# Performance work log

Measured on AMD Instinct MI355X. Metric: run time of the kernel, lower is better.

## Reference

```python
import jax, jax.numpy as jnp
import numpy as np

N_EMBD = 1024
N_HEAD = 16
B, T = 1, 4096
EPS = 1e-5


def layer_norm(x, w):
    mu = jnp.mean(x, axis=-1, keepdims=True)
    var = jnp.var(x, axis=-1, keepdims=True)
    return (x - mu) / jnp.sqrt(var + EPS) * w


def setup_inputs() -> dict:
    key = jax.random.key(0)
    ks = jax.random.split(key, 6)
    s = 0.02
    return {
        "x": jax.random.normal(ks[0], (B, T, N_EMBD), dtype=jnp.float32),
        "w_qkv": jax.random.normal(ks[1], (N_EMBD, 3 * N_EMBD), dtype=jnp.float32) * s,
        "w_attn_proj": jax.random.normal(ks[2], (N_EMBD, N_EMBD), dtype=jnp.float32) * s,
        "w_fc": jax.random.normal(ks[3], (N_EMBD, 4 * N_EMBD), dtype=jnp.float32) * s,
        "w_mlp_proj": jax.random.normal(ks[4], (4 * N_EMBD, N_EMBD), dtype=jnp.float32) * s,
        "ln1_w": jnp.ones((N_EMBD,), dtype=jnp.float32),
        "ln2_w": jnp.ones((N_EMBD,), dtype=jnp.float32),
    }


def reference(x, w_qkv, w_attn_proj, w_fc, w_mlp_proj, ln1_w, ln2_w):
    Bq, Tq, C = x.shape
    hs = C // N_HEAD

    # --- attention branch (pre-norm) ---
    h = layer_norm(x, ln1_w)
    qkv = h @ w_qkv  # [B,T,3C]
    q, k, v = jnp.split(qkv, 3, axis=-1)
    q = q.reshape(Bq, Tq, N_HEAD, hs).transpose(0, 2, 1, 3)  # [B,H,T,hs]
    k = k.reshape(Bq, Tq, N_HEAD, hs).transpose(0, 2, 1, 3)
    v = v.reshape(Bq, Tq, N_HEAD, hs).transpose(0, 2, 1, 3)

    scores = jnp.einsum("bhqd,bhkd->bhqk", q, k) * (1.0 / jnp.sqrt(jnp.float32(hs)))
    causal = jnp.tril(jnp.ones((Tq, Tq), dtype=bool))
    scores = jnp.where(causal, scores, -jnp.inf)
    weights = jax.nn.softmax(scores, axis=-1)  # dropout=0 -> identity
    out = jnp.einsum("bhqk,bhkd->bhqd", weights, v)
    out = out.transpose(0, 2, 1, 3).reshape(Bq, Tq, C)
    x = x + out @ w_attn_proj

    # --- MLP branch (pre-norm) ---
    h = layer_norm(x, ln2_w)
    h = jax.nn.gelu(h @ w_fc, approximate=False)  # nn.GELU default is exact
    x = x + h @ w_mlp_proj
    return x
```

## Files before the change

### kernel.cpp

```cpp
#include <hip/hip_runtime.h>
#include <cstdint>

typedef __attribute__((ext_vector_type(8))) short short8;
typedef __attribute__((ext_vector_type(4))) float f32x4;

__device__ __forceinline__ float b2f(unsigned short u) {
    return __uint_as_float(((unsigned int)u) << 16);
}
__device__ __forceinline__ unsigned short f2b(float f) {
    unsigned int u = __float_as_uint(f);
    u += 0x7FFFu + ((u >> 16) & 1u);
    return (unsigned short)(u >> 16);
}

__global__ __launch_bounds__(256) void k_transpose_all(
        const float* __restrict__ w0, const float* __restrict__ w1,
        const float* __restrict__ w2, const float* __restrict__ w3,
        unsigned short* __restrict__ o0, unsigned short* __restrict__ o1,
        unsigned short* __restrict__ o2, unsigned short* __restrict__ o3) {
    __shared__ float tile[32][33];
    int b = blockIdx.x;
    const float* w; unsigned short* o; int K, N, nx, tb;
    if (b < 3072)      { w = w0; o = o0; K = 1024; N = 3072; nx = 96;  tb = b; }
    else if (b < 4096) { w = w1; o = o1; K = 1024; N = 1024; nx = 32;  tb = b - 3072; }
    else if (b < 8192) { w = w2; o = o2; K = 1024; N = 4096; nx = 128; tb = b - 4096; }
    else               { w = w3; o = o3; K = 4096; N = 1024; nx = 32;  tb = b - 8192; }
    int n0 = (tb % nx) * 32, k0 = (tb / nx) * 32;
    int tx = threadIdx.x, ty = threadIdx.y;
#pragma unroll
    for (int i = 0; i < 4; i++)
        tile[ty + 8 * i][tx] = w[(size_t)(k0 + ty + 8 * i) * N + n0 + tx];
    __syncthreads();
#pragma unroll
    for (int i = 0; i < 4; i++)
        o[(size_t)(n0 + ty + 8 * i) * K + k0 + tx] = f2b(tile[tx][ty + 8 * i]);
}

__global__ __launch_bounds__(256) void k_layernorm(
        const float* __restrict__ x, const float* __restrict__ w,
        unsigned short* __restrict__ out) {
    int row = blockIdx.x, tid = threadIdx.x;
    const float4* xr = (const float4*)(x + (size_t)row * 1024);
    float4 v = xr[tid];
    float s  = v.x + v.y + v.z + v.w;
    float ss = v.x * v.x + v.y * v.y + v.z * v.z + v.w * v.w;
#pragma unroll
    for (int off = 32; off >= 1; off >>= 1) {
        s  += __shfl_down(s, off);
        ss += __shfl_down(ss, off);
    }
    __shared__ float red[10];
    if ((tid & 63) == 0) { red[tid >> 6] = s; red[4 + (tid >> 6)] = ss; }
    __syncthreads();
    if (tid == 0) {
        float S  = red[0] + red[1] + red[2] + red[3];
        float SS = red[4] + red[5] + red[6] + red[7];
        float mu  = S * (1.0f / 1024.0f);
        float var = SS * (1.0f / 1024.0f) - mu * mu;
        red[8] = mu; red[9] = rsqrtf(var + 1e-5f);
    }
    __syncthreads();
    float mu = red[8], rs = red[9];
    float4 wv = ((const float4*)w)[tid];
    ushort4 pk;
    pk.x = f2b((v.x - mu) * rs * wv.x);
    pk.y = f2b((v.y - mu) * rs * wv.y);
    pk.z = f2b((v.z - mu) * rs * wv.z);
    pk.w = f2b((v.w - mu) * rs * wv.w);
    *(ushort4*)(out + (size_t)row * 1024 + tid * 4) = pk;
}

__global__ __launch_bounds__(256) void k_reduce(
        const float* __restrict__ res, const float* __restrict__ p0,
        const float* __restrict__ p1, float* __restrict__ out, int n4) {
    int i = blockIdx.x * 256 + threadIdx.x;
    if (i < n4) {
        float4 a = ((const float4*)res)[i];
        float4 b = ((const float4*)p0)[i];
        float4 c = ((const float4*)p1)[i];
        a.x += b.x + c.x; a.y += b.y + c.y; a.z += b.z + c.z; a.w += b.w + c.w;
        ((float4*)out)[i] = a;
    }
}

template <int EPI, int TM, int TN, int MINW>
__global__ __launch_bounds__(256, MINW) void k_gemm_bt(
        const unsigned short* __restrict__ A, const unsigned short* __restrict__ BT,
        const float* __restrict__ RES, void* __restrict__ OUT,
        int M, int N, int K) {
    constexpr int WT = (TM == 128) ? 64 : 32;
    constexpr int MI = WT / 16;
    constexpr int NA = TM / 32, NB = TN / 32;
    __shared__ __align__(16) unsigned short As[TM * 64];
    __shared__ __align__(16) unsigned short Bs[TN * 64];
    int tid  = threadIdx.x;
    int lane = tid & 63, wave = tid >> 6;
    int quad = lane >> 4, qr = lane & 15;
    int wm_off = (wave >> 1) * WT;
    int wn_off = (wave & 1) * WT;
    int m0 = blockIdx.y * TM, n0 = blockIdx.x * TN;
    int ks = K / gridDim.z;
    int kbeg = blockIdx.z * ks;
    int r0 = tid >> 3;
    int c0 = (tid & 7) * 8;
    int cs = 8 * (((tid & 7) + (r0 & 7)) & 7);
    int cswz[2];
#pragma unroll
    for (int kk = 0; kk < 2; kk++) cswz[kk] = 8 * (((kk * 4) + quad + (qr & 7)) & 7);

    const unsigned short* Ap = A  + (size_t)(m0 + r0) * K + kbeg + c0;
    const unsigned short* Bp = BT + (size_t)(n0 + r0) * K + kbeg + c0;
    const size_t sA = (size_t)32 * K;

    uint4 pa0, pa1, pa2, pa3, pb0, pb1, pb2, pb3;
    pa0 = *(const uint4*)(Ap);
    pa1 = *(const uint4*)(Ap + sA);
    if constexpr (NA == 4) {
        pa2 = *(const uint4*)(Ap + 2 * sA);
        pa3 = *(const uint4*)(Ap + 3 * sA);
    }
    pb0 = *(const uint4*)(Bp);
    pb1 = *(const uint4*)(Bp + sA);
    if constexpr (NB == 4) {
        pb2 = *(const uint4*)(Bp + 2 * sA);
        pb3 = *(const uint4*)(Bp + 3 * sA);
    }

    f32x4 acc[MI][MI] = {};
    for (int k0 = 0; k0 < ks; k0 += 64) {
        __syncthreads();
        *(uint4*)&As[(r0)      * 64 + cs] = pa0;
        *(uint4*)&As[(32 + r0) * 64 + cs] = pa1;
        if constexpr (NA == 4) {
            *(uint4*)&As[(64 + r0) * 64 + cs] = pa2;
            *(uint4*)&As[(96 + r0) * 64 + cs] = pa3;
        }
        *(uint4*)&Bs[(r0)      * 64 + cs] = pb0;
        *(uint4*)&Bs[(32 + r0) * 64 + cs] = pb1;
        if constexpr (NB == 4) {
            *(uint4*)&Bs[(64 + r0) * 64 + cs] = pb2;
            *(uint4*)&Bs[(96 + r0) * 64 + cs] = pb3;
        }
        __syncthreads();
        if (k0 + 64 < ks) {
            int k = k0 + 64;
            pa0 = *(const uint4*)(Ap + k);
            pa1 = *(const uint4*)(Ap + sA + k);
            if constexpr (NA == 4) {
                pa2 = *(const uint4*)(Ap + 2 * sA + k);
                pa3 = *(const uint4*)(Ap + 3 * sA + k);
            }
            pb0 = *(const uint4*)(Bp + k);
            pb1 = *(const uint4*)(Bp + sA + k);
            if constexpr (NB == 4) {
                pb2 = *(const uint4*)(Bp + 2 * sA + k);
                pb3 = *(const uint4*)(Bp + 3 * sA + k);
            }
        }
#pragma unroll
        for (int kk = 0; kk < 2; kk++) {
            short8 af[MI], bfr[MI];
#pragma unroll
            for (int i = 0; i < MI; i++) af[i]  = *(const short8*)&As[(wm_off + i * 16 + qr) * 64 + cswz[kk]];
#pragma unroll
            for (int j = 0; j < MI; j++) bfr[j] = *(const short8*)&Bs[(wn_off + j * 16 + qr) * 64 + cswz[kk]];
#pragma unroll
            for (int i = 0; i < MI; i++)
#pragma unroll
                for (int j = 0; j < MI; j++)
                    acc[i][j] = __builtin_amdgcn_mfma_f32_16x16x32_bf16(af[i], bfr[j], acc[i][j], 0, 0, 0);
        }
    }
    float* outz = (EPI == 0) ? ((float*)OUT + (size_t)blockIdx.z * M * N) : (float*)OUT;
#pragma unroll
    for (int i = 0; i < MI; i++) {
#pragma unroll
        for (int j = 0; j < MI; j++) {
#pragma unroll
            for (int r = 0; r < 4; r++) {
                int row = m0 + wm_off + i * 16 + quad * 4 + r;
                int col = n0 + wn_off + j * 16 + qr;
                size_t idx = (size_t)row * N + col;
                float v = acc[i][j][r];
                if (EPI == 0)      outz[idx] = v;
                else if (EPI == 1) ((unsigned short*)OUT)[idx] = f2b(v);
                else if (EPI == 2) ((float*)OUT)[idx] = RES[idx] + v;
                else {
                    float u = v * fmaf(v * v, 0.035677408f, 0.79788456f);
                    float e = fminf(u * 2.885390082f, 80.0f);
                    float t = exp2f(e);
                    float g = v * t / (t + 1.0f);
                    ((unsigned short*)OUT)[idx] = f2b(g);
                }
            }
        }
    }
}

__global__ __launch_bounds__(256) void k_attn(
        const unsigned short* __restrict__ qkv, unsigned short* __restrict__ out) {
    __shared__ unsigned short Ks[128][72];
    __shared__ unsigned short Vt[64][136];
    __shared__ unsigned short Ps[4][16][136];

    const float C1 = 0.18033688f;
    const float C2 = 5.77078016f;

    int l = blockIdx.x;
    int h = l & 15;
    int qb = 63 - (l >> 4);
    int q0 = qb * 64;

    int tid = threadIdx.x;
    int wave = tid >> 6, lane = tid & 63;
    int lane16 = lane & 15, quad = lane >> 4;

    {
        int srow = tid >> 2, sc0 = (tid & 3) * 16;
        size_t base = (size_t)(q0 + srow) * 3072 + h * 64 + sc0;
        *(uint4*)&Ks[srow][sc0]     = *(const uint4*)&qkv[base];
        *(uint4*)&Ks[srow][sc0 + 8] = *(const uint4*)&qkv[base + 8];
    }
    __syncthreads();
    short8 aq0 = *(const short8*)&Ks[wave * 16 + lane16][quad * 8];
    short8 aq1 = *(const short8*)&Ks[wave * 16 + lane16][32 + quad * 8];

    f32x4 Oacc[4] = {};
    float l_part[4] = {0.f, 0.f, 0.f, 0.f};

    int srow = tid >> 1, sc0 = (tid & 1) * 32;
    int vk = (lane & 31) * 2;
    int d0 = wave * 16 + (lane >> 5) * 8;

    uint4 pk0, pk1, pk2, pk3, pv0, pv1, pv2, pv3;
    {
        size_t base = (size_t)srow * 3072 + 1024 + h * 64 + sc0;
        pk0 = *(const uint4*)&qkv[base];
        pk1 = *(const uint4*)&qkv[base + 8];
        pk2 = *(const uint4*)&qkv[base + 16];
        pk3 = *(const uint4*)&qkv[base + 24];
        size_t vb0 = (size_t)vk * 3072 + 2048 + h * 64 + d0;
        pv0 = *(const uint4*)&qkv[vb0];
        pv1 = *(const uint4*)&qkv[vb0 + 3072];
        size_t vb1 = (size_t)(64 + vk) * 3072 + 2048 + h * 64 + d0;
        pv2 = *(const uint4*)&qkv[vb1];
        pv3 = *(const uint4*)&qkv[vb1 + 3072];
    }

    for (int kc = 0; kc <= qb; kc += 2) {
        __syncthreads();
        {
            *(uint4*)&Ks[srow][sc0]      = pk0;
            *(uint4*)&Ks[srow][sc0 + 8]  = pk1;
            *(uint4*)&Ks[srow][sc0 + 16] = pk2;
            *(uint4*)&Ks[srow][sc0 + 24] = pk3;
        }
        {
            const unsigned short* pe0 = (const unsigned short*)&pv0;
            const unsigned short* po0 = (const unsigned short*)&pv1;
            const unsigned short* pe1 = (const unsigned short*)&pv2;
            const unsigned short* po1 = (const unsigned short*)&pv3;
#pragma unroll
            for (int j = 0; j < 8; j++) {
                *(uint32_t*)&Vt[d0 + j][vk]      = (uint32_t)pe0[j] | ((uint32_t)po0[j] << 16);
                *(uint32_t*)&Vt[d0 + j][64 + vk] = (uint32_t)pe1[j] | ((uint32_t)po1[j] << 16);
            }
        }
        __syncthreads();

        if (kc + 2 <= qb) {
            size_t base = (size_t)((kc + 2) * 64 + srow) * 3072 + 1024 + h * 64 + sc0;
            pk0 = *(const uint4*)&qkv[base];
            pk1 = *(const uint4*)&qkv[base + 8];
            pk2 = *(const uint4*)&qkv[base + 16];
            pk3 = *(const uint4*)&qkv[base + 24];
            size_t vb0 = (size_t)((kc + 2) * 64 + vk) * 3072 + 2048 + h * 64 + d0;
            pv0 = *(const uint4*)&qkv[vb0];
            pv1 = *(const uint4*)&qkv[vb0 + 3072];
            size_t vb1 = (size_t)((kc + 3) * 64 + vk) * 3072 + 2048 + h * 64 + d0;
            pv2 = *(const uint4*)&qkv[vb1];
            pv3 = *(const uint4*)&qkv[vb1 + 3072];
        }

        f32x4 sacc[8] = {};
#pragma unroll
        for (int kt = 0; kt < 8; kt++) {
            short8 bk0 = *(const short8*)&Ks[kt * 16 + lane16][quad * 8];
            short8 bk1 = *(const short8*)&Ks[kt * 16 + lane16][32 + quad * 8];
            sacc[kt] = __builtin_amdgcn_mfma_f32_16x16x32_bf16(aq0, bk0, sacc[kt], 0, 0, 0);
            sacc[kt] = __builtin_amdgcn_mfma_f32_16x16x32_bf16(aq1, bk1, sacc[kt], 0, 0, 0);
        }

        bool domask = (kc + 2 > qb);
#pragma unroll
        for (int r = 0; r < 4; r++) {
            int qrow = q0 + wave * 16 + quad * 4 + r;
#pragma unroll
            for (int kt = 0; kt < 8; kt++) {
                float s = sacc[kt][r];
                if (domask) {
                    int key = kc * 64 + kt * 16 + lane16;
                    s = (key <= qrow) ? s : -__builtin_inff();
                }
                float p = exp2f(fmaf(s, C1, -C2));
                l_part[r] += p;
                Ps[wave][quad * 4 + r][kt * 16 + lane16] =
                    (unsigned short)(__float_as_uint(p) >> 16);
            }
        }

#pragma unroll
        for (int s = 0; s < 4; s++) {
            short8 ap = *(const short8*)&Ps[wave][lane16][s * 32 + quad * 8];
#pragma unroll
            for (int dt = 0; dt < 4; dt++) {
                short8 bv = *(const short8*)&Vt[dt * 16 + lane16][s * 32 + quad * 8];
                Oacc[dt] = __builtin_amdgcn_mfma_f32_16x16x32_bf16(ap, bv, Oacc[dt], 0, 0, 0);
            }
        }
    }

    float invl[4];
#pragma unroll
    for (int r = 0; r < 4; r++) {
        float lf = l_part[r];
        lf += __shfl_xor(lf, 1);
        lf += __shfl_xor(lf, 2);
        lf += __shfl_xor(lf, 4);
        lf += __shfl_xor(lf, 8);
        invl[r] = 1.0f / lf;
    }
#pragma unroll
    for (int dt = 0; dt < 4; dt++) {
#pragma unroll
        for (int r = 0; r < 4; r++) {
            int qrow = q0 + wave * 16 + quad * 4 + r;
            out[(size_t)qrow * 1024 + h * 64 + dt * 16 + lane16] = f2b(Oacc[dt][r] * invl[r]);
        }
    }
}

extern "C" void kernel_launch(void* const* d_in, const int* in_sizes, int n_in,
                              void* d_out, int out_size, void* d_ws, size_t ws_size,
                              hipStream_t stream) {
    const float* x      = (const float*)d_in[0];
    const float* w_qkv  = (const float*)d_in[1];
    const float* w_attn = (const float*)d_in[2];
    const float* w_fc   = (const float*)d_in[3];
    const float* w_mlp  = (const float*)d_in[4];
    const float* ln1w   = (const float*)d_in[5];
    const float* ln2w   = (const float*)d_in[6];

    char* ws = (char*)d_ws;
    unsigned short* h      = (unsigned short*)(ws + 0);
    unsigned short* wqkvT  = (unsigned short*)(ws + 8388608);
    unsigned short* wattnT = (unsigned short*)(ws + 14680064);
    unsigned short* wfcT   = (unsigned short*)(ws + 16777216);
    unsigned short* wmlpT  = (unsigned short*)(ws + 25165824);
    unsigned short* qkv    = (unsigned short*)(ws + 33554432);
    unsigned short* attno  = (unsigned short*)(ws + 58720256);
    float*          x2     = (float*)(ws + 67108864);
    unsigned short* fcact  = (unsigned short*)(ws + 83886080);
    float* pA = (float*)(ws + 83886080);
    float* pM = (float*)(ws + 33554432);
    float* outF = (float*)d_out;

    k_transpose_all<<<12288, dim3(32, 8), 0, stream>>>(
        w_qkv, w_attn, w_fc, w_mlp, wqkvT, wattnT, wfcT, wmlpT);

    k_layernorm<<<4096, 256, 0, stream>>>(x, ln1w, h);
    k_gemm_bt<1, 128, 128, 3><<<dim3(24, 32), 256, 0, stream>>>(h, wqkvT, nullptr, qkv, 4096, 3072, 1024);
    k_attn<<<1024, 256, 0, stream>>>(qkv, attno);
    k_gemm_bt<0, 128, 128, 3><<<dim3(8, 32, 2), 256, 0, stream>>>(attno, wattnT, nullptr, pA, 4096, 1024, 1024);
    k_reduce<<<4096, 256, 0, stream>>>(x, pA, pA + 4194304, x2, 1048576);
    k_layernorm<<<4096, 256, 0, stream>>>(x2, ln2w, h);
    k_gemm_bt<3, 128, 128, 3><<<dim3(32, 32), 256, 0, stream>>>(h, wfcT, nullptr, fcact, 4096, 4096, 1024);
    k_gemm_bt<0, 128, 128, 3><<<dim3(8, 32, 2), 256, 0, stream>>>(fcact, wmlpT, nullptr, pM, 4096, 1024, 4096);
    k_reduce<<<4096, 256, 0, stream>>>(x2, pM, pM + 4194304, outF, 1048576);
}
```

Measured before the change: 356.9 us.

## Keep attention probabilities in registers by transposing QK MFMA and permuting V layout

Swaps the MFMA operands in the QK^T product so each lane holds scores for one query row across consecutive keys. The probabilities can then be packed straight into the A operand of the PV MFMA, with no round-trip through LDS. The V transpose store is permuted so its key order matches this register layout. The Ps shared buffer and its stores and reloads are removed, the row-sum reduction is simplified, and launch bounds request 4 blocks per CU. The cost is more intricate index mapping and possible register-pressure limits from the occupancy hint.

```diff
diff --git a/kernel.cpp b/kernel.cpp
--- a/kernel.cpp
+++ b/kernel.cpp
@@ -3,6 +3,7 @@
 
 typedef __attribute__((ext_vector_type(8))) short short8;
 typedef __attribute__((ext_vector_type(4))) float f32x4;
+typedef __attribute__((ext_vector_type(4))) unsigned int u32x4;
 
 __device__ __forceinline__ float b2f(unsigned short u) {
     return __uint_as_float(((unsigned int)u) << 16);
@@ -197,11 +198,10 @@
     }
 }
 
-__global__ __launch_bounds__(256) void k_attn(
+__global__ __launch_bounds__(256, 4) void k_attn(
         const unsigned short* __restrict__ qkv, unsigned short* __restrict__ out) {
     __shared__ unsigned short Ks[128][72];
     __shared__ unsigned short Vt[64][136];
-    __shared__ unsigned short Ps[4][16][136];
 
     const float C1 = 0.18033688f;
     const float C2 = 5.77078016f;
@@ -214,6 +214,7 @@
     int tid = threadIdx.x;
     int wave = tid >> 6, lane = tid & 63;
     int lane16 = lane & 15, quad = lane >> 4;
+    int qrow = q0 + wave * 16 + lane16;
 
     {
         int srow = tid >> 2, sc0 = (tid & 3) * 16;
@@ -226,11 +227,14 @@
     short8 aq1 = *(const short8*)&Ks[wave * 16 + lane16][32 + quad * 8];
 
     f32x4 Oacc[4] = {};
-    float l_part[4] = {0.f, 0.f, 0.f, 0.f};
+    float lsum = 0.f;
 
     int srow = tid >> 1, sc0 = (tid & 1) * 32;
     int vk = (lane & 31) * 2;
     int d0 = wave * 16 + (lane >> 5) * 8;
+    int u  = lane & 15;
+    int tt = ((u & 6) << 1) | ((u & 8) >> 2) | (u & 1);
+    int dstc = (lane & 16) * 2 + 2 * tt;
 
     uint4 pk0, pk1, pk2, pk3, pv0, pv1, pv2, pv3;
     {
@@ -262,8 +266,8 @@
             const unsigned short* po1 = (const unsigned short*)&pv3;
 #pragma unroll
             for (int j = 0; j < 8; j++) {
-                *(uint32_t*)&Vt[d0 + j][vk]      = (uint32_t)pe0[j] | ((uint32_t)po0[j] << 16);
-                *(uint32_t*)&Vt[d0 + j][64 + vk] = (uint32_t)pe1[j] | ((uint32_t)po1[j] << 16);
+                *(uint32_t*)&Vt[d0 + j][dstc]      = (uint32_t)pe0[j] | ((uint32_t)po0[j] << 16);
+                *(uint32_t*)&Vt[d0 + j][64 + dstc] = (uint32_t)pe1[j] | ((uint32_t)po1[j] << 16);
             }
         }
         __syncthreads();
@@ -287,55 +291,59 @@
         for (int kt = 0; kt < 8; kt++) {
             short8 bk0 = *(const short8*)&Ks[kt * 16 + lane16][quad * 8];
             short8 bk1 = *(const short8*)&Ks[kt * 16 + lane16][32 + quad * 8];
-            sacc[kt] = __builtin_amdgcn_mfma_f32_16x16x32_bf16(aq0, bk0, sacc[kt], 0, 0, 0);
-            sacc[kt] = __builtin_amdgcn_mfma_f32_16x16x32_bf16(aq1, bk1, sacc[kt], 0, 0, 0);
+            sacc[kt] = __builtin_amdgcn_mfma_f32_16x16x32_bf16(bk0, aq0, sacc[kt], 0, 0, 0);
+            sacc[kt] = __builtin_amdgcn_mfma_f32_16x16x32_bf16(bk1, aq1, sacc[kt], 0, 0, 0);
         }
 
         bool domask = (kc + 2 > qb);
-#pragma unroll
-        for (int r = 0; r < 4; r++) {
-            int qrow = q0 + wave * 16 + quad * 4 + r;
-#pragma unroll
-            for (int kt = 0; kt < 8; kt++) {
-                float s = sacc[kt][r];
-                if (domask) {
-                    int key = kc * 64 + kt * 16 + lane16;
-                    s = (key <= qrow) ? s : -__builtin_inff();
+        short8 ap[4];
+#pragma unroll
+        for (int s = 0; s < 4; s++) {
+            u32x4 w;
+#pragma unroll
+            for (int hh = 0; hh < 2; hh++) {
+                int kt = 2 * s + hh;
+                float pr[4];
+#pragma unroll
+                for (int r = 0; r < 4; r++) {
+                    float sc = sacc[kt][r];
+                    if (domask) {
+                        int key = kc * 64 + kt * 16 + quad * 4 + r;
+                        sc = (key <= qrow) ? sc : -__builtin_inff();
+                    }
+                    float p = exp2f(fmaf(sc, C1, -C2));
+                    lsum += p;
+                    pr[r] = p;
                 }
-                float p = exp2f(fmaf(s, C1, -C2));
-                l_part[r] += p;
-                Ps[wave][quad * 4 + r][kt * 16 + lane16] =
-                    (unsigned short)(__float_as_uint(p) >> 16);
-            }
+                uint32_t w0 = (__float_as_uint(pr[0]) >> 16) | (__float_as_uint(pr[1]) & 0xFFFF0000u);
+                uint32_t w1 = (__float_as_uint(pr[2]) >> 16) | (__float_as_uint(pr[3]) & 0xFFFF0000u);
+                if (hh == 0) { w.x = w0; w.y = w1; } else { w.z = w0; w.w = w1; }
+            }
+            ap[s] = __builtin_bit_cast(short8, w);
         }
 
 #pragma unroll
         for (int s = 0; s < 4; s++) {
-            short8 ap = *(const short8*)&Ps[wave][lane16][s * 32 + quad * 8];
 #pragma unroll
             for (int dt = 0; dt < 4; dt++) {
                 short8 bv = *(const short8*)&Vt[dt * 16 + lane16][s * 32 + quad * 8];
-                Oacc[dt] = __builtin_amdgcn_mfma_f32_16x16x32_bf16(ap, bv, Oacc[dt], 0, 0, 0);
-            }
-        }
-    }
-
+                Oacc[dt] = __builtin_amdgcn_mfma_f32_16x16x32_bf16(ap[s], bv, Oacc[dt], 0, 0, 0);
+            }
+        }
+    }
+
+    float lf = lsum;
+    lf += __shfl_xor(lf, 16);
+    lf += __shfl_xor(lf, 32);
     float invl[4];
 #pragma unroll
-    for (int r = 0; r < 4; r++) {
-        float lf = l_part[r];
-        lf += __shfl_xor(lf, 1);
-        lf += __shfl_xor(lf, 2);
-        lf += __shfl_xor(lf, 4);
-        lf += __shfl_xor(lf, 8);
-        invl[r] = 1.0f / lf;
-    }
+    for (int r = 0; r < 4; r++) invl[r] = 1.0f / __shfl(lf, quad * 4 + r);
 #pragma unroll
     for (int dt = 0; dt < 4; dt++) {
 #pragma unroll
         for (int r = 0; r < 4; r++) {
-            int qrow = q0 + wave * 16 + quad * 4 + r;
-            out[(size_t)qrow * 1024 + h * 64 + dt * 16 + lane16] = f2b(Oacc[dt][r] * invl[r]);
+            int qr_out = q0 + wave * 16 + quad * 4 + r;
+            out[(size_t)qr_out * 1024 + h * 64 + dt * 16 + lane16] = f2b(Oacc[dt][r] * invl[r]);
         }
     }
 }
```

After: 373.6 us. 4.7% more time.

## Split long causal attention rows across two blocks and fuse residual-reduce with layernorm

Applied to the files above, without the earlier changes.

Query blocks in the upper half of the sequence now have their key range split into two segments, each handled by its own workgroup. Each segment writes unnormalized fp32 partial outputs and row sums, and a new combine kernel merges them into bf16. This balances work across the 1536 blocks for causal attention, at the cost of extra fp32 traffic and one more launch. The residual-add reduce and the second layernorm are also fused into one kernel, which saves a launch and a re-read of x2.

```diff
diff --git a/kernel.cpp b/kernel.cpp
--- a/kernel.cpp
+++ b/kernel.cpp
@@ -68,6 +68,47 @@
     pk.z = f2b((v.z - mu) * rs * wv.z);
     pk.w = f2b((v.w - mu) * rs * wv.w);
     *(ushort4*)(out + (size_t)row * 1024 + tid * 4) = pk;
+}
+
+__global__ __launch_bounds__(256) void k_reduce_ln(
+        const float* __restrict__ res, const float* __restrict__ p0,
+        const float* __restrict__ p1, const float* __restrict__ w,
+        float* __restrict__ xout, unsigned short* __restrict__ hout) {
+    int row = blockIdx.x, tid = threadIdx.x;
+    size_t i = (size_t)row * 256 + tid;
+    float4 a = ((const float4*)res)[i];
+    float4 b = ((const float4*)p0)[i];
+    float4 c = ((const float4*)p1)[i];
+    float4 v;
+    v.x = a.x + b.x + c.x; v.y = a.y + b.y + c.y;
+    v.z = a.z + b.z + c.z; v.w = a.w + b.w + c.w;
+    ((float4*)xout)[i] = v;
+    float s  = v.x + v.y + v.z + v.w;
+    float ss = v.x * v.x + v.y * v.y + v.z * v.z + v.w * v.w;
+#pragma unroll
+    for (int off = 32; off >= 1; off >>= 1) {
+        s  += __shfl_down(s, off);
+        ss += __shfl_down(ss, off);
+    }
+    __shared__ float red[10];
+    if ((tid & 63) == 0) { red[tid >> 6] = s; red[4 + (tid >> 6)] = ss; }
+    __syncthreads();
+    if (tid == 0) {
+        float S  = red[0] + red[1] + red[2] + red[3];
+        float SS = red[4] + red[5] + red[6] + red[7];
+        float mu  = S * (1.0f / 1024.0f);
+        float var = SS * (1.0f / 1024.0f) - mu * mu;
+        red[8] = mu; red[9] = rsqrtf(var + 1e-5f);
+    }
+    __syncthreads();
+    float mu = red[8], rs = red[9];
+    float4 wv = ((const float4*)w)[tid];
+    ushort4 pk;
+    pk.x = f2b((v.x - mu) * rs * wv.x);
+    pk.y = f2b((v.y - mu) * rs * wv.y);
+    pk.z = f2b((v.z - mu) * rs * wv.z);
+    pk.w = f2b((v.w - mu) * rs * wv.w);
+    *(ushort4*)(hout + (size_t)row * 1024 + tid * 4) = pk;
 }
 
 __global__ __launch_bounds__(256) void k_reduce(
@@ -198,7 +239,8 @@
 }
 
 __global__ __launch_bounds__(256) void k_attn(
-        const unsigned short* __restrict__ qkv, unsigned short* __restrict__ out) {
+        const unsigned short* __restrict__ qkv, unsigned short* __restrict__ out,
+        float* __restrict__ pO, float* __restrict__ pL) {
     __shared__ unsigned short Ks[128][72];
     __shared__ unsigned short Vt[64][136];
     __shared__ unsigned short Ps[4][16][136];
@@ -208,8 +250,15 @@
 
     int l = blockIdx.x;
     int h = l & 15;
-    int qb = 63 - (l >> 4);
+    int u = l >> 4;
+    int k_ = u / 6, r_ = u - 6 * k_;
+    int qb, seg, split;
+    if (r_ < 4)      { qb = (r_ < 2 ? 63 : 62) - 2 * k_; seg = 1 - (r_ & 1); split = 1; }
+    else             { qb = (r_ == 4 ? 31 : 30) - 2 * k_; seg = 0; split = 0; }
     int q0 = qb * 64;
+    int nc = (qb >> 1) + 1;
+    int kcbeg = (split && seg == 1) ? 2 * (nc >> 1) : 0;
+    int kcend = (split && seg == 0) ? 2 * (nc >> 1) : 2 * nc;
 
     int tid = threadIdx.x;
     int wave = tid >> 6, lane = tid & 63;
@@ -234,20 +283,20 @@
 
     uint4 pk0, pk1, pk2, pk3, pv0, pv1, pv2, pv3;
     {
-        size_t base = (size_t)srow * 3072 + 1024 + h * 64 + sc0;
+        size_t base = (size_t)(kcbeg * 64 + srow) * 3072 + 1024 + h * 64 + sc0;
         pk0 = *(const uint4*)&qkv[base];
         pk1 = *(const uint4*)&qkv[base + 8];
         pk2 = *(const uint4*)&qkv[base + 16];
         pk3 = *(const uint4*)&qkv[base + 24];
-        size_t vb0 = (size_t)vk * 3072 + 2048 + h * 64 + d0;
+        size_t vb0 = (size_t)(kcbeg * 64 + vk) * 3072 + 2048 + h * 64 + d0;
         pv0 = *(const uint4*)&qkv[vb0];
         pv1 = *(const uint4*)&qkv[vb0 + 3072];
-        size_t vb1 = (size_t)(64 + vk) * 3072 + 2048 + h * 64 + d0;
+        size_t vb1 = (size_t)(kcbeg * 64 + 64 + vk) * 3072 + 2048 + h * 64 + d0;
         pv2 = *(const uint4*)&qkv[vb1];
         pv3 = *(const uint4*)&qkv[vb1 + 3072];
     }
 
-    for (int kc = 0; kc <= qb; kc += 2) {
+    for (int kc = kcbeg; kc < kcend; kc += 2) {
         __syncthreads();
         {
             *(uint4*)&Ks[srow][sc0]      = pk0;
@@ -268,7 +317,7 @@
         }
         __syncthreads();
 
-        if (kc + 2 <= qb) {
+        if (kc + 2 < kcend) {
             size_t base = (size_t)((kc + 2) * 64 + srow) * 3072 + 1024 + h * 64 + sc0;
             pk0 = *(const uint4*)&qkv[base];
             pk1 = *(const uint4*)&qkv[base + 8];
@@ -320,7 +369,7 @@
         }
     }
 
-    float invl[4];
+    float lfull[4];
 #pragma unroll
     for (int r = 0; r < 4; r++) {
         float lf = l_part[r];
@@ -328,15 +377,62 @@
         lf += __shfl_xor(lf, 2);
         lf += __shfl_xor(lf, 4);
         lf += __shfl_xor(lf, 8);
-        invl[r] = 1.0f / lf;
-    }
-#pragma unroll
-    for (int dt = 0; dt < 4; dt++) {
-#pragma unroll
-        for (int r = 0; r < 4; r++) {
-            int qrow = q0 + wave * 16 + quad * 4 + r;
-            out[(size_t)qrow * 1024 + h * 64 + dt * 16 + lane16] = f2b(Oacc[dt][r] * invl[r]);
-        }
+        lfull[r] = lf;
+    }
+
+    if (!split) {
+#pragma unroll
+        for (int dt = 0; dt < 4; dt++) {
+#pragma unroll
+            for (int r = 0; r < 4; r++) {
+                int qrow = q0 + wave * 16 + quad * 4 + r;
+                out[(size_t)qrow * 1024 + h * 64 + dt * 16 + lane16] =
+                    f2b(Oacc[dt][r] * (1.0f / lfull[r]));
+            }
+        }
+    } else {
+        size_t pb = ((((size_t)seg * 16 + h) * 32 + (qb - 32)) * 64) * 64;
+#pragma unroll
+        for (int dt = 0; dt < 4; dt++) {
+#pragma unroll
+            for (int r = 0; r < 4; r++) {
+                int q = wave * 16 + quad * 4 + r;
+                pO[pb + (size_t)q * 64 + dt * 16 + lane16] = Oacc[dt][r];
+            }
+        }
+        if (lane16 == 0) {
+            size_t lb = (((size_t)seg * 16 + h) * 32 + (qb - 32)) * 64;
+#pragma unroll
+            for (int r = 0; r < 4; r++)
+                pL[lb + wave * 16 + quad * 4 + r] = lfull[r];
+        }
+    }
+}
+
+__global__ __launch_bounds__(256) void k_attn_combine(
+        const float* __restrict__ pO, const float* __restrict__ pL,
+        unsigned short* __restrict__ out) {
+    int b = blockIdx.x;
+    int h = b & 15, qi = b >> 4;
+    int q0 = (32 + qi) * 64;
+    int t = threadIdx.x;
+    int q = t >> 2, dd = (t & 3) * 16;
+    size_t b0 = ((((size_t)0 * 16 + h) * 32 + qi) * 64 + q) * 64 + dd;
+    size_t b1 = ((((size_t)1 * 16 + h) * 32 + qi) * 64 + q) * 64 + dd;
+    float l0 = pL[(((size_t)0 * 16 + h) * 32 + qi) * 64 + q];
+    float l1 = pL[(((size_t)1 * 16 + h) * 32 + qi) * 64 + q];
+    float inv = 1.0f / (l0 + l1);
+    unsigned short* op = out + (size_t)(q0 + q) * 1024 + h * 64 + dd;
+#pragma unroll
+    for (int j = 0; j < 4; j++) {
+        float4 a = ((const float4*)(pO + b0))[j];
+        float4 c = ((const float4*)(pO + b1))[j];
+        ushort4 pk;
+        pk.x = f2b((a.x + c.x) * inv);
+        pk.y = f2b((a.y + c.y) * inv);
+        pk.z = f2b((a.z + c.z) * inv);
+        pk.w = f2b((a.w + c.w) * inv);
+        *(ushort4*)(op + j * 4) = pk;
     }
 }
 
@@ -361,6 +457,8 @@
     unsigned short* attno  = (unsigned short*)(ws + 58720256);
     float*          x2     = (float*)(ws + 67108864);
     unsigned short* fcact  = (unsigned short*)(ws + 83886080);
+    float* pO = (float*)(ws + 83886080);
+    float* pL = (float*)(ws + 100663296);
     float* pA = (float*)(ws + 83886080);
     float* pM = (float*)(ws + 33554432);
     float* outF = (float*)d_out;
@@ -370,10 +468,10 @@
 
     k_layernorm<<<4096, 256, 0, stream>>>(x, ln1w, h);
     k_gemm_bt<1, 128, 128, 3><<<dim3(24, 32), 256, 0, stream>>>(h, wqkvT, nullptr, qkv, 4096, 3072, 1024);
-    k_attn<<<1024, 256, 0, stream>>>(qkv, attno);
+    k_attn<<<1536, 256, 0, stream>>>(qkv, attno, pO, pL);
+    k_attn_combine<<<512, 256, 0, stream>>>(pO, pL, attno);
     k_gemm_bt<0, 128, 128, 3><<<dim3(8, 32, 2), 256, 0, stream>>>(attno, wattnT, nullptr, pA, 4096, 1024, 1024);
-    k_reduce<<<4096, 256, 0, stream>>>(x, pA, pA + 4194304, x2, 1048576);
-    k_layernorm<<<4096, 256, 0, stream>>>(x2, ln2w, h);
+    k_reduce_ln<<<4096, 256, 0, stream>>>(x, pA, pA + 4194304, ln2w, x2, h);
     k_gemm_bt<3, 128, 128, 3><<<dim3(32, 32), 256, 0, stream>>>(h, wfcT, nullptr, fcact, 4096, 4096, 1024);
     k_gemm_bt<0, 128, 128, 3><<<dim3(8, 32, 2), 256, 0, stream>>>(fcact, wmlpT, nullptr, pM, 4096, 1024, 4096);
     k_reduce<<<4096, 256, 0, stream>>>(x2, pM, pM + 4194304, outF, 1048576);
```

After: 380.7 us. +6.7%, slower.

## Add 256x256 8-wave pipelined GEMM with direct-to-LDS loads; fuse reduce+LayerNorm

Applied to the files above, without the earlier changes.

Adds a new GEMM kernel using 256x256 tiles, 512 threads, double-buffered LDS filled by global_load_lds with XOR swizzle, and phased interleaving of loads with MFMA under setprio. It is used for the QKV and FC projections in place of the 128x128 kernel. Separately, the residual split-K reduction is fused with the second LayerNorm, removing one pass over the activations. The large tile gives fewer blocks (192 and 256 on a 256-CU part), which risks underfilling the GPU, and the hand-tuned waitcnt and barrier schedule is fragile.

```diff
diff --git a/kernel.cpp b/kernel.cpp
--- a/kernel.cpp
+++ b/kernel.cpp
@@ -11,6 +11,11 @@
     unsigned int u = __float_as_uint(f);
     u += 0x7FFFu + ((u >> 16) & 1u);
     return (unsigned short)(u >> 16);
+}
+__device__ __forceinline__ void gload16(const unsigned short* g, unsigned short* l) {
+    __builtin_amdgcn_global_load_lds(
+        (const __attribute__((address_space(1))) void*)g,
+        (__attribute__((address_space(3))) void*)l, 16, 0, 0);
 }
 
 __global__ __launch_bounds__(256) void k_transpose_all(
@@ -68,6 +73,47 @@
     pk.z = f2b((v.z - mu) * rs * wv.z);
     pk.w = f2b((v.w - mu) * rs * wv.w);
     *(ushort4*)(out + (size_t)row * 1024 + tid * 4) = pk;
+}
+
+__global__ __launch_bounds__(256) void k_reduce_ln(
+        const float* __restrict__ res, const float* __restrict__ p0,
+        const float* __restrict__ p1, const float* __restrict__ w,
+        float* __restrict__ xout, unsigned short* __restrict__ hout) {
+    int row = blockIdx.x, tid = threadIdx.x;
+    size_t i = (size_t)row * 256 + tid;
+    float4 a = ((const float4*)res)[i];
+    float4 b = ((const float4*)p0)[i];
+    float4 c = ((const float4*)p1)[i];
+    float4 v;
+    v.x = a.x + b.x + c.x; v.y = a.y + b.y + c.y;
+    v.z = a.z + b.z + c.z; v.w = a.w + b.w + c.w;
+    ((float4*)xout)[i] = v;
+    float s  = v.x + v.y + v.z + v.w;
+    float ss = v.x * v.x + v.y * v.y + v.z * v.z + v.w * v.w;
+#pragma unroll
+    for (int off = 32; off >= 1; off >>= 1) {
+        s  += __shfl_down(s, off);
+        ss += __shfl_down(ss, off);
+    }
+    __shared__ float red[10];
+    if ((tid & 63) == 0) { red[tid >> 6] = s; red[4 + (tid >> 6)] = ss; }
+    __syncthreads();
+    if (tid == 0) {
+        float S  = red[0] + red[1] + red[2] + red[3];
+        float SS = red[4] + red[5] + red[6] + red[7];
+        float mu  = S * (1.0f / 1024.0f);
+        float var = SS * (1.0f / 1024.0f) - mu * mu;
+        red[8] = mu; red[9] = rsqrtf(var + 1e-5f);
+    }
+    __syncthreads();
+    float mu = red[8], rs = red[9];
+    float4 wv = ((const float4*)w)[tid];
+    ushort4 pk;
+    pk.x = f2b((v.x - mu) * rs * wv.x);
+    pk.y = f2b((v.y - mu) * rs * wv.y);
+    pk.z = f2b((v.z - mu) * rs * wv.z);
+    pk.w = f2b((v.w - mu) * rs * wv.w);
+    *(ushort4*)(hout + (size_t)row * 1024 + tid * 4) = pk;
 }
 
 __global__ __launch_bounds__(256) void k_reduce(
@@ -197,6 +243,119 @@
     }
 }
 
+template <int EPI>
+__global__ __launch_bounds__(512, 2) void k_gemm_8p(
+        const unsigned short* __restrict__ A, const unsigned short* __restrict__ BT,
+        void* __restrict__ OUT, int M, int N, int K) {
+    __shared__ __align__(16) unsigned short As[2][256 * 64];
+    __shared__ __align__(16) unsigned short Bs[2][256 * 64];
+    int tid = threadIdx.x;
+    int lane = tid & 63, wave = tid >> 6;
+    int quad = lane >> 4, qr = lane & 15;
+    int wr = wave >> 2, wc = wave & 3;
+    int m0 = blockIdx.y * 256, n0 = blockIdx.x * 256;
+    int nk = K / 64;
+
+    int srow = tid >> 3, sblk = tid & 7;
+    int scol = 8 * ((sblk - (srow & 7)) & 7);
+    const unsigned short* Ag = A  + (size_t)(m0 + srow) * K + scol;
+    const unsigned short* Bg = BT + (size_t)(n0 + srow) * K + scol;
+    const size_t rstep = (size_t)64 * K;
+
+    int cswz[2];
+#pragma unroll
+    for (int kk = 0; kk < 2; kk++) cswz[kk] = 8 * (((kk * 4) + quad + (qr & 7)) & 7);
+
+    auto stageA = [&](int buf, int half, int kt) {
+        int k = (kt < nk ? kt : 0) * 64;
+#pragma unroll
+        for (int rr = 0; rr < 2; rr++) {
+            int r4 = half * 2 + rr;
+            gload16(Ag + (size_t)r4 * rstep + k, &As[buf][r4 * 4096 + wave * 512]);
+        }
+    };
+    auto stageB = [&](int buf, int half, int kt) {
+        int k = (kt < nk ? kt : 0) * 64;
+#pragma unroll
+        for (int rr = 0; rr < 2; rr++) {
+            int r4 = half * 2 + rr;
+            gload16(Bg + (size_t)r4 * rstep + k, &Bs[buf][r4 * 4096 + wave * 512]);
+        }
+    };
+
+    f32x4 acc[8][4] = {};
+    stageA(0, 0, 0); stageA(0, 1, 0); stageB(0, 0, 0); stageB(0, 1, 0);
+    stageA(1, 0, 1); stageA(1, 1, 1); stageB(1, 0, 1); stageB(1, 1, 1);
+    asm volatile("s_waitcnt vmcnt(8)" ::: "memory");
+    __builtin_amdgcn_s_barrier();
+
+    short8 bf[4][2];
+    for (int t = 0; t < nk; t += 2) {
+#pragma unroll
+        for (int ph = 0; ph < 8; ph++) {
+            const int B = ph >> 2;
+            const int p = ph & 3;
+            if (p == 0) {
+#pragma unroll
+                for (int j = 0; j < 4; j++)
+#pragma unroll
+                    for (int kk = 0; kk < 2; kk++)
+                        bf[j][kk] = *(const short8*)&Bs[B][(wc * 64 + j * 16 + qr) * 64 + cswz[kk]];
+            }
+            short8 af[2][2];
+#pragma unroll
+            for (int i2 = 0; i2 < 2; i2++)
+#pragma unroll
+                for (int kk = 0; kk < 2; kk++)
+                    af[i2][kk] = *(const short8*)&As[B][(wr * 128 + (p * 2 + i2) * 16 + qr) * 64 + cswz[kk]];
+            if (ph == 0)      { if (t) stageA(1, 0, t + 1); }
+            else if (ph == 1) { if (t) stageA(1, 1, t + 1); stageB(0, 0, t + 2); }
+            else if (ph == 2) { stageB(0, 1, t + 2); }
+            else if (ph == 4) { stageA(0, 0, t + 2); }
+            else if (ph == 5) { stageA(0, 1, t + 2); stageB(1, 0, t + 3); }
+            else if (ph == 6) { stageB(1, 1, t + 3); }
+            __builtin_amdgcn_s_barrier();
+            asm volatile("s_waitcnt lgkmcnt(0)" ::: "memory");
+            __builtin_amdgcn_sched_barrier(0);
+            __builtin_amdgcn_s_setprio(1);
+#pragma unroll
+            for (int i2 = 0; i2 < 2; i2++)
+#pragma unroll
+                for (int kk = 0; kk < 2; kk++)
+#pragma unroll
+                    for (int j = 0; j < 4; j++)
+                        acc[p * 2 + i2][j] = __builtin_amdgcn_mfma_f32_16x16x32_bf16(
+                            af[i2][kk], bf[j][kk], acc[p * 2 + i2][j], 0, 0, 0);
+            __builtin_amdgcn_s_setprio(0);
+            if (p == 3) asm volatile("s_waitcnt vmcnt(4)" ::: "memory");
+            __builtin_amdgcn_s_barrier();
+        }
+    }
+    asm volatile("s_waitcnt vmcnt(0)" ::: "memory");
+
+#pragma unroll
+    for (int i = 0; i < 8; i++) {
+#pragma unroll
+        for (int j = 0; j < 4; j++) {
+#pragma unroll
+            for (int r = 0; r < 4; r++) {
+                int row = m0 + wr * 128 + i * 16 + quad * 4 + r;
+                int col = n0 + wc * 64 + j * 16 + qr;
+                size_t idx = (size_t)row * N + col;
+                float v = acc[i][j][r];
+                if (EPI == 1) ((unsigned short*)OUT)[idx] = f2b(v);
+                else {
+                    float u = v * fmaf(v * v, 0.035677408f, 0.79788456f);
+                    float e = fminf(u * 2.885390082f, 80.0f);
+                    float tt = exp2f(e);
+                    float g = v * tt / (tt + 1.0f);
+                    ((unsigned short*)OUT)[idx] = f2b(g);
+                }
+            }
+        }
+    }
+}
+
 __global__ __launch_bounds__(256) void k_attn(
         const unsigned short* __restrict__ qkv, unsigned short* __restrict__ out) {
     __shared__ unsigned short Ks[128][72];
@@ -369,12 +528,11 @@
         w_qkv, w_attn, w_fc, w_mlp, wqkvT, wattnT, wfcT, wmlpT);
 
     k_layernorm<<<4096, 256, 0, stream>>>(x, ln1w, h);
-    k_gemm_bt<1, 128, 128, 3><<<dim3(24, 32), 256, 0, stream>>>(h, wqkvT, nullptr, qkv, 4096, 3072, 1024);
+    k_gemm_8p<1><<<dim3(12, 16), 512, 0, stream>>>(h, wqkvT, qkv, 4096, 3072, 1024);
     k_attn<<<1024, 256, 0, stream>>>(qkv, attno);
     k_gemm_bt<0, 128, 128, 3><<<dim3(8, 32, 2), 256, 0, stream>>>(attno, wattnT, nullptr, pA, 4096, 1024, 1024);
-    k_reduce<<<4096, 256, 0, stream>>>(x, pA, pA + 4194304, x2, 1048576);
-    k_layernorm<<<4096, 256, 0, stream>>>(x2, ln2w, h);
-    k_gemm_bt<3, 128, 128, 3><<<dim3(32, 32), 256, 0, stream>>>(h, wfcT, nullptr, fcact, 4096, 4096, 1024);
+    k_reduce_ln<<<4096, 256, 0, stream>>>(x, pA, pA + 4194304, ln2w, x2, h);
+    k_gemm_8p<3><<<dim3(16, 16), 512, 0, stream>>>(h, wfcT, fcact, 4096, 4096, 1024);
     k_gemm_bt<0, 128, 128, 3><<<dim3(8, 32, 2), 256, 0, stream>>>(fcact, wmlpT, nullptr, pM, 4096, 1024, 4096);
     k_reduce<<<4096, 256, 0, stream>>>(x2, pM, pM + 4194304, outF, 1048576);
 }
```

Result: slower. 364.1 us (+2.0%).
